# Optimization experiments

Measured on AMD Instinct MI355X. Metric: run time of the kernel, lower is better.

Reference implementation:

```python
import jax, jax.numpy as jnp
import numpy as np

B, L, D, H, NB = 64, 30, 512, 8, 6
AS, MT = 18, 4096
T = 3 * L
HD = D // H
EPS = 1e-3  # keras LayerNormalization default epsilon
CONV_FEAT = 7 * 7 * 64  # 84 ->(8,s4) 20 ->(4,s2) 9 ->(3,s1) 7


def setup_inputs() -> dict:
    key = jax.random.key(0)
    ks = iter(jax.random.split(key, 64))
    r = lambda *s: jax.random.normal(next(ks), s, jnp.float32) * 0.02
    inp = {
        'rtgs': jax.random.normal(next(ks), (B, L, 1), jnp.float32),
        'states': jax.random.uniform(next(ks), (B, L, 84, 84, 4), jnp.float32) * 255.0,
        'actions': jax.random.randint(next(ks), (B, L, 1), 0, AS),
        'timesteps': jax.random.randint(next(ks), (B, 1, 1), 0, MT + 1),
        # rtg embedding
        'W_rtg': r(1, D), 'b_rtg': r(D),
        # state conv stem (HWIO)
        'conv1_w': r(8, 8, 4, 32), 'conv1_b': r(32),
        'conv2_w': r(4, 4, 32, 64), 'conv2_b': r(64),
        'conv3_w': r(3, 3, 64, 64), 'conv3_b': r(64),
        'dense_s_w': r(CONV_FEAT, D), 'dense_s_b': r(D),
        # action embedding table
        'emb_a': r(AS, D),
        # positional embeddings
        'abs_pos': r(1, MT + 1, D), 'rel_pos': r(1, T + 1, D),
        # decoder blocks (stacked over NB)
        'ln1_g': 1.0 + r(NB, D), 'ln1_b': r(NB, D),
        'Wk': r(NB, D, D), 'bk': r(NB, D),
        'Wq': r(NB, D, D), 'bq': r(NB, D),
        'Wv': r(NB, D, D), 'bv': r(NB, D),
        'ln2_g': 1.0 + r(NB, D), 'ln2_b': r(NB, D),
        'W1': r(NB, D, 4 * D), 'b1': r(NB, 4 * D),
        'W2': r(NB, 4 * D, D), 'b2': r(NB, D),
        # final norm + head (no bias)
        'lnf_g': 1.0 + r(D), 'lnf_b': r(D),
        'W_head': r(D, AS),
    }
    return inp


def _conv(x, w, b, stride):
    y = jax.lax.conv_general_dilated(x, w, (stride, stride), 'VALID',
                                     dimension_numbers=('NHWC', 'HWIO', 'NHWC'))
    return jax.nn.relu(y + b)


def _layernorm(x, g, b):
    m = x.mean(-1, keepdims=True)
    v = ((x - m) ** 2).mean(-1, keepdims=True)
    return (x - m) / jnp.sqrt(v + EPS) * g + b


def _attn(x, Wk, bk, Wq, bq, Wv, bv):
    Bx, Tx, C = x.shape
    split = lambda z: z.reshape(Bx, Tx, H, HD).transpose(0, 2, 1, 3)  # (B,H,T,hd)
    k, q, v = split(x @ Wk + bk), split(x @ Wq + bq), split(x @ Wv + bv)
    # NOTE: faithful to source: scores = K @ Q^T (not Q @ K^T)
    s = jnp.einsum('bhid,bhjd->bhij', k, q) / jnp.sqrt(jnp.float32(HD))
    mask = jnp.tril(jnp.ones((Tx, Tx), bool))
    s = jnp.where(mask, s, -jnp.inf)
    w = jax.nn.softmax(s, axis=-1)
    o = jnp.einsum('bhij,bhjd->bhid', w, v)
    return o.transpose(0, 2, 1, 3).reshape(Bx, Tx, C)


def reference(rtgs, states, actions, timesteps, W_rtg, b_rtg,
              conv1_w, conv1_b, conv2_w, conv2_b, conv3_w, conv3_b,
              dense_s_w, dense_s_b, emb_a, abs_pos, rel_pos,
              ln1_g, ln1_b, Wk, bk, Wq, bq, Wv, bv,
              ln2_g, ln2_b, W1, b1, W2, b2, lnf_g, lnf_b, W_head):
    # embeddings
    rtg_e = jnp.tanh(rtgs @ W_rtg + b_rtg)                       # (B,L,D)
    s = states.reshape(B * L, 84, 84, 4) / 255.0
    s = _conv(s, conv1_w, conv1_b, 4)
    s = _conv(s, conv2_w, conv2_b, 2)
    s = _conv(s, conv3_w, conv3_b, 1)
    st_e = jnp.tanh(s.reshape(B, L, -1) @ dense_s_w + dense_s_b)  # (B,L,D)
    a_e = jnp.tanh(emb_a[actions[..., 0]])                        # (B,L,D)
    # positional: abs gathered at start timestep + relative
    abs_e = abs_pos[0][timesteps[:, 0, 0]][:, None, :]            # (B,1,D)
    pos = rel_pos[:, :T, :] + abs_e                               # (B,3L,D)
    # interleave (rtg, state, action) per timestep
    tokens = jnp.stack([rtg_e, st_e, a_e], axis=2).reshape(B, T, D)
    x = tokens + pos
    for i in range(NB):
        h = _layernorm(x, ln1_g[i], ln1_b[i])
        x = x + _attn(h, Wk[i], bk[i], Wq[i], bq[i], Wv[i], bv[i])
        h = _layernorm(x, ln2_g[i], ln2_b[i])
        x = x + jax.nn.gelu(h @ W1[i] + b1[i], approximate=False) @ W2[i] + b2[i]
    x = _layernorm(x, lnf_g, lnf_b)
    logits = x @ W_head                                           # (B,3L,AS)
    return logits[:, 1::3, :]                                     # state positions -> (B,L,AS)
```

## Files before the change

### kernel.cpp

```cpp
#include <hip/hip_runtime.h>
#include <hip/hip_bf16.h>

typedef __attribute__((ext_vector_type(8))) __bf16 bf16x8;
typedef __attribute__((ext_vector_type(4))) float f32x4;

#define ACT_NONE 0
#define ACT_RELU 1
#define ACT_GELU 2
#define ACT_TANH 3
#define OUT_F32 0
#define OUT_BF16 1
#define OUT_ADD 2

template<int MODE, int K>
__device__ __forceinline__ size_t a_rowbase(int m) {
  if constexpr (MODE == 0) {
    return (size_t)m * K;
  } else if constexpr (MODE == 1) {
    int img = m / 400; int p = m - img * 400; int oy = p / 20; int ox = p - oy * 20;
    return (size_t)img * 28224 + oy * 1344 + ox * 16;
  } else if constexpr (MODE == 2) {
    int img = m / 81; int p = m - img * 81; int oy = p / 9; int ox = p - oy * 9;
    return (size_t)img * 12800 + oy * 1280 + ox * 64;
  } else {
    int img = m / 49; int p = m - img * 49; int oy = p / 7; int ox = p - oy * 7;
    return (size_t)img * 5184 + oy * 576 + ox * 64;
  }
}
template<int MODE>
__device__ __forceinline__ int a_koff(int k) {
  if constexpr (MODE == 0) return k;
  else if constexpr (MODE == 1) return (k >> 5) * 336 + (k & 31);
  else if constexpr (MODE == 2) return (k >> 7) * 640 + ((k >> 5) & 3) * 32 + (k & 31);
  else { int ky = k / 192; int r = k - ky * 192; return ky * 576 + r; }
}

template<bool F32>
__device__ __forceinline__ bf16x8 ld8(const void* p) {
  if constexpr (F32) {
    const float* f = (const float*)p;
    float4 a = *(const float4*)f;
    float4 b = *(const float4*)(f + 4);
    bf16x8 r;
    r[0] = (__bf16)a.x; r[1] = (__bf16)a.y; r[2] = (__bf16)a.z; r[3] = (__bf16)a.w;
    r[4] = (__bf16)b.x; r[5] = (__bf16)b.y; r[6] = (__bf16)b.z; r[7] = (__bf16)b.w;
    return r;
  } else {
    return *(const bf16x8*)p;
  }
}

template<int MODE, bool AF32, int NREAL, int K, int ACT, int OUTM, int LDC>
__global__ __launch_bounds__(256) void gemm_k(const void* __restrict__ Av,
                                              const __bf16* __restrict__ BT,
                                              const float* __restrict__ bias,
                                              void* __restrict__ C) {
  constexpr int LDAS = 48;
  __shared__ __bf16 As[128 * LDAS];
  __shared__ __bf16 Bs[128 * LDAS];
  const __bf16* Ab = (const __bf16*)Av;
  const float* Af = (const float*)Av;
  const int tid = threadIdx.x;
  const int wave = tid >> 6, lane = tid & 63;
  const int quad = lane >> 4, l16 = lane & 15;
  const int wr = wave >> 1, wc = wave & 1;
  const int m0 = blockIdx.x * 128, n0 = blockIdx.y * 128;

  const int c0 = tid, c1 = tid + 256;
  const int r0 = c0 >> 2, k0o = (c0 & 3) * 8;
  const int r1 = c1 >> 2, k1o = (c1 & 3) * 8;
  const size_t ar0 = a_rowbase<MODE, K>(m0 + r0);
  const size_t ar1 = a_rowbase<MODE, K>(m0 + r1);
  const size_t br0 = (size_t)(n0 + r0) * K;
  const size_t br1 = (size_t)(n0 + r1) * K;

  auto aptr = [&](size_t idx) -> const void* {
    if constexpr (AF32) return (const void*)(Af + idx);
    else return (const void*)(Ab + idx);
  };

  f32x4 acc[4][4] = {};
  bf16x8 av0 = ld8<AF32>(aptr(ar0 + a_koff<MODE>(k0o)));
  bf16x8 av1 = ld8<AF32>(aptr(ar1 + a_koff<MODE>(k1o)));
  bf16x8 bv0 = *(const bf16x8*)(BT + br0 + k0o);
  bf16x8 bv1 = *(const bf16x8*)(BT + br1 + k1o);

  constexpr int NK = K / 32;
  for (int kt = 0; kt < NK; ++kt) {
    __syncthreads();
    *(bf16x8*)&As[r0 * LDAS + k0o] = av0;
    *(bf16x8*)&As[r1 * LDAS + k1o] = av1;
    *(bf16x8*)&Bs[r0 * LDAS + k0o] = bv0;
    *(bf16x8*)&Bs[r1 * LDAS + k1o] = bv1;
    __syncthreads();
    if (kt + 1 < NK) {
      const int kb = (kt + 1) * 32;
      av0 = ld8<AF32>(aptr(ar0 + a_koff<MODE>(kb + k0o)));
      av1 = ld8<AF32>(aptr(ar1 + a_koff<MODE>(kb + k1o)));
      bv0 = *(const bf16x8*)(BT + br0 + kb + k0o);
      bv1 = *(const bf16x8*)(BT + br1 + kb + k1o);
    }
    bf16x8 af[4], bfv[4];
#pragma unroll
    for (int mt = 0; mt < 4; ++mt)
      af[mt] = *(const bf16x8*)&As[(wr * 64 + mt * 16 + l16) * LDAS + quad * 8];
#pragma unroll
    for (int nt = 0; nt < 4; ++nt)
      bfv[nt] = *(const bf16x8*)&Bs[(wc * 64 + nt * 16 + l16) * LDAS + quad * 8];
#pragma unroll
    for (int mt = 0; mt < 4; ++mt)
#pragma unroll
      for (int nt = 0; nt < 4; ++nt)
        acc[mt][nt] = __builtin_amdgcn_mfma_f32_16x16x32_bf16(af[mt], bfv[nt], acc[mt][nt], 0, 0, 0);
  }

#pragma unroll
  for (int nt = 0; nt < 4; ++nt) {
    const int col = n0 + wc * 64 + nt * 16 + l16;
    if (col < NREAL) {
      const float bvl = bias[col];
#pragma unroll
      for (int mt = 0; mt < 4; ++mt) {
#pragma unroll
        for (int r = 0; r < 4; ++r) {
          const int row = m0 + wr * 64 + mt * 16 + quad * 4 + r;
          float v = acc[mt][nt][r] + bvl;
          if constexpr (ACT == ACT_RELU) v = fmaxf(v, 0.f);
          else if constexpr (ACT == ACT_GELU) v = 0.5f * v * (1.f + erff(v * 0.70710678118f));
          else if constexpr (ACT == ACT_TANH) v = tanhf(v);
          const size_t off = (size_t)row * LDC + col;
          if constexpr (OUTM == OUT_F32) ((float*)C)[off] = v;
          else if constexpr (OUTM == OUT_BF16) ((__bf16*)C)[off] = (__bf16)v;
          else ((float*)C)[off] += v;
        }
      }
    }
  }
}

template<typename TO>
__global__ void transpose_pad(const float* __restrict__ src, TO* __restrict__ dst,
                              int R, int C, int Cpad, long long sz, long long dz, float scale) {
  src += blockIdx.z * sz; dst += blockIdx.z * dz;
  __shared__ float t[32][33];
  const int tx = threadIdx.x, ty = threadIdx.y;
  const int r0 = blockIdx.x * 32, c0 = blockIdx.y * 32;
  for (int i = ty; i < 32; i += 8) {
    int r = r0 + i, c = c0 + tx;
    t[i][tx] = (r < R && c < C) ? src[(size_t)r * C + c] : 0.f;
  }
  __syncthreads();
  for (int i = ty; i < 32; i += 8) {
    int c = c0 + i, r = r0 + tx;
    if (c < Cpad && r < R)
      dst[(size_t)c * R + r] = (c < C) ? (TO)(t[tx][i] * scale) : (TO)0.f;
  }
}

__global__ void biascat_k(const float* bk, const float* bq, const float* bv, float* dst) {
  const int i = blockIdx.x;
  for (int d = threadIdx.x; d < 512; d += 256) {
    dst[i * 1536 + d] = bk[i * 512 + d];
    dst[i * 1536 + 512 + d] = bq[i * 512 + d];
    dst[i * 1536 + 1024 + d] = bv[i * 512 + d];
  }
}

__global__ void embed_k(const float* __restrict__ rtgs, const int* __restrict__ actions,
                        const int* __restrict__ timesteps, const float* __restrict__ W_rtg,
                        const float* __restrict__ b_rtg, const float* __restrict__ emb_a,
                        const float* __restrict__ abs_pos, const float* __restrict__ rel_pos,
                        const float* __restrict__ ste, float* __restrict__ x) {
  const int idx = blockIdx.x * 256 + threadIdx.x;
  const int d = idx & 511; const int rb = idx >> 9;
  const int b = rb / 90, t = rb - b * 90;
  const int l = t / 3, r = t - l * 3;
  const float pos = rel_pos[t * 512 + d] + abs_pos[(size_t)timesteps[b] * 512 + d];
  float tok;
  if (r == 0) tok = tanhf(rtgs[b * 30 + l] * W_rtg[d] + b_rtg[d]);
  else if (r == 1) tok = ste[(size_t)(b * 30 + l) * 512 + d];
  else tok = tanhf(emb_a[actions[b * 30 + l] * 512 + d]);
  x[idx] = tok + pos;
}

__global__ __launch_bounds__(256) void ln_k(const float* __restrict__ x, const float* __restrict__ g,
                                            const float* __restrict__ bb, __bf16* __restrict__ h) {
  const int row = blockIdx.x * 4 + (threadIdx.x >> 6);
  const int lane = threadIdx.x & 63;
  const float* xr = x + (size_t)row * 512;
  float4 a = *(const float4*)&xr[lane * 8];
  float4 c = *(const float4*)&xr[lane * 8 + 4];
  float vv[8] = {a.x, a.y, a.z, a.w, c.x, c.y, c.z, c.w};
  float s = 0.f, q = 0.f;
#pragma unroll
  for (int j = 0; j < 8; ++j) { s += vv[j]; q += vv[j] * vv[j]; }
  for (int o = 32; o; o >>= 1) { s += __shfl_xor(s, o); q += __shfl_xor(q, o); }
  const float mean = s * (1.f / 512.f);
  const float var = q * (1.f / 512.f) - mean * mean;
  const float rstd = rsqrtf(var + 1e-3f);
  float4 g1 = *(const float4*)&g[lane * 8];
  float4 g2 = *(const float4*)&g[lane * 8 + 4];
  float4 b1 = *(const float4*)&bb[lane * 8];
  float4 b2 = *(const float4*)&bb[lane * 8 + 4];
  float gg[8] = {g1.x, g1.y, g1.z, g1.w, g2.x, g2.y, g2.z, g2.w};
  float bbv[8] = {b1.x, b1.y, b1.z, b1.w, b2.x, b2.y, b2.z, b2.w};
  bf16x8 ov;
#pragma unroll
  for (int j = 0; j < 8; ++j)
    ov[j] = (__bf16)((vv[j] - mean) * rstd * gg[j] + bbv[j]);
  *(bf16x8*)&h[(size_t)row * 512 + lane * 8] = ov;
}

__global__ __launch_bounds__(256) void attn_k(const __bf16* __restrict__ qkv, float* __restrict__ x) {
  __shared__ __align__(16) char smem[64512];
  __bf16* kS = (__bf16*)smem;
  __bf16* qS = (__bf16*)(smem + 13824);
  __bf16* wS = (__bf16*)smem;
  float* sS = (float*)(smem + 27648);
  __bf16* vT = (__bf16*)(smem + 27648);

  const int tid = threadIdx.x;
  const int b = blockIdx.x >> 3, h = blockIdx.x & 7;
  const int wave = tid >> 6, lane = tid & 63, quad = lane >> 4, l16 = lane & 15;
  const size_t rowbase = (size_t)b * 90 * 1536 + h * 64;

  for (int c = tid; c < 768; c += 256) {
    const int t = c >> 3, d8 = (c & 7) * 8;
    bf16x8 kv, qv;
#pragma unroll
    for (int j = 0; j < 8; ++j) { kv[j] = (__bf16)0.f; qv[j] = (__bf16)0.f; }
    if (t < 90) {
      const __bf16* src = qkv + rowbase + (size_t)t * 1536 + d8;
      kv = *(const bf16x8*)src;
      qv = *(const bf16x8*)(src + 512);
    }
    *(bf16x8*)&kS[t * 72 + d8] = kv;
    *(bf16x8*)&qS[t * 72 + d8] = qv;
  }
  __syncthreads();

  for (int tt = wave; tt < 36; tt += 4) {
    const int it = tt / 6, jt = tt - it * 6;
    f32x4 acc = {0.f, 0.f, 0.f, 0.f};
#pragma unroll
    for (int ks = 0; ks < 2; ++ks) {
      bf16x8 af = *(const bf16x8*)&kS[(it * 16 + l16) * 72 + ks * 32 + quad * 8];
      bf16x8 bq = *(const bf16x8*)&qS[(jt * 16 + l16) * 72 + ks * 32 + quad * 8];
      acc = __builtin_amdgcn_mfma_f32_16x16x32_bf16(af, bq, acc, 0, 0, 0);
    }
    const int col = jt * 16 + l16;
#pragma unroll
    for (int r = 0; r < 4; ++r) {
      const int row = it * 16 + quad * 4 + r;
      sS[row * 96 + col] = (col <= row && col < 90) ? acc[r] * 0.125f : -1e30f;
    }
  }
  __syncthreads();

  for (int row = wave; row < 96; row += 4) {
    const float e0 = sS[row * 96 + lane];
    const float e1 = (lane < 32) ? sS[row * 96 + 64 + lane] : -1e30f;
    float m = fmaxf(e0, e1);
    for (int o = 32; o; o >>= 1) m = fmaxf(m, __shfl_xor(m, o));
    const float p0 = __expf(e0 - m);
    const float p1 = (lane < 32) ? __expf(e1 - m) : 0.f;
    float s = p0 + p1;
    for (int o = 32; o; o >>= 1) s += __shfl_xor(s, o);
    const float inv = 1.f / s;
    wS[row * 104 + lane] = (__bf16)(p0 * inv);
    if (lane < 32) wS[row * 104 + 64 + lane] = (__bf16)(p1 * inv);
  }
  __syncthreads();

  for (int c = tid; c < 768; c += 256) {
    const int t = c >> 3, d8 = (c & 7) * 8;
    bf16x8 vv;
#pragma unroll
    for (int j = 0; j < 8; ++j) vv[j] = (__bf16)0.f;
    if (t < 90) vv = *(const bf16x8*)(qkv + rowbase + (size_t)t * 1536 + 1024 + d8);
#pragma unroll
    for (int j = 0; j < 8; ++j) vT[(d8 + j) * 104 + t] = vv[j];
  }
  __syncthreads();

  for (int tt = wave; tt < 24; tt += 4) {
    const int it = tt >> 2, dt = tt & 3;
    f32x4 acc = {0.f, 0.f, 0.f, 0.f};
#pragma unroll
    for (int ks = 0; ks < 3; ++ks) {
      bf16x8 aw = *(const bf16x8*)&wS[(it * 16 + l16) * 104 + ks * 32 + quad * 8];
      bf16x8 bv = *(const bf16x8*)&vT[(dt * 16 + l16) * 104 + ks * 32 + quad * 8];
      acc = __builtin_amdgcn_mfma_f32_16x16x32_bf16(aw, bv, acc, 0, 0, 0);
    }
    const int d = dt * 16 + l16;
#pragma unroll
    for (int r = 0; r < 4; ++r) {
      const int i = it * 16 + quad * 4 + r;
      if (i < 90) {
        float* p = x + (size_t)(b * 90 + i) * 512 + h * 64 + d;
        *p += acc[r];
      }
    }
  }
}

__global__ __launch_bounds__(64) void head_k(const float* __restrict__ x, const float* __restrict__ g,
                                             const float* __restrict__ bb, const float* __restrict__ whT,
                                             float* __restrict__ out) {
  const int m = blockIdx.x;
  const int b = m / 30, l = m - b * 30;
  const float* xr = x + (size_t)(b * 90 + 3 * l + 1) * 512;
  const int lane = threadIdx.x;
  float4 a = *(const float4*)&xr[lane * 8];
  float4 c = *(const float4*)&xr[lane * 8 + 4];
  float vv[8] = {a.x, a.y, a.z, a.w, c.x, c.y, c.z, c.w};
  float s = 0.f, q = 0.f;
#pragma unroll
  for (int j = 0; j < 8; ++j) { s += vv[j]; q += vv[j] * vv[j]; }
  for (int o = 32; o; o >>= 1) { s += __shfl_xor(s, o); q += __shfl_xor(q, o); }
  const float mean = s * (1.f / 512.f);
  const float var = q * (1.f / 512.f) - mean * mean;
  const float rstd = rsqrtf(var + 1e-3f);
  float4 g1 = *(const float4*)&g[lane * 8];
  float4 g2 = *(const float4*)&g[lane * 8 + 4];
  float4 b1 = *(const float4*)&bb[lane * 8];
  float4 b2 = *(const float4*)&bb[lane * 8 + 4];
  float gg[8] = {g1.x, g1.y, g1.z, g1.w, g2.x, g2.y, g2.z, g2.w};
  float bbv[8] = {b1.x, b1.y, b1.z, b1.w, b2.x, b2.y, b2.z, b2.w};
#pragma unroll
  for (int j = 0; j < 8; ++j)
    vv[j] = (vv[j] - mean) * rstd * gg[j] + bbv[j];
  for (int aa = 0; aa < 18; ++aa) {
    float4 w1v = *(const float4*)&whT[aa * 512 + lane * 8];
    float4 w2v = *(const float4*)&whT[aa * 512 + lane * 8 + 4];
    float ww[8] = {w1v.x, w1v.y, w1v.z, w1v.w, w2v.x, w2v.y, w2v.z, w2v.w};
    float d = 0.f;
#pragma unroll
    for (int j = 0; j < 8; ++j) d += vv[j] * ww[j];
    for (int o = 32; o; o >>= 1) d += __shfl_xor(d, o);
    if (lane == 0) out[m * 18 + aa] = d;
  }
}

extern "C" void kernel_launch(void* const* d_in, const int* in_sizes, int n_in,
                              void* d_out, int out_size, void* d_ws, size_t ws_size,
                              hipStream_t stream) {
  const float* rtgs = (const float*)d_in[0];
  const float* states = (const float*)d_in[1];
  const int* actions = (const int*)d_in[2];
  const int* timesteps = (const int*)d_in[3];
  const float* W_rtg = (const float*)d_in[4];
  const float* b_rtg = (const float*)d_in[5];
  const float* conv1_w = (const float*)d_in[6];
  const float* conv1_b = (const float*)d_in[7];
  const float* conv2_w = (const float*)d_in[8];
  const float* conv2_b = (const float*)d_in[9];
  const float* conv3_w = (const float*)d_in[10];
  const float* conv3_b = (const float*)d_in[11];
  const float* dense_s_w = (const float*)d_in[12];
  const float* dense_s_b = (const float*)d_in[13];
  const float* emb_a = (const float*)d_in[14];
  const float* abs_pos = (const float*)d_in[15];
  const float* rel_pos = (const float*)d_in[16];
  const float* ln1_g = (const float*)d_in[17];
  const float* ln1_b = (const float*)d_in[18];
  const float* Wk = (const float*)d_in[19];
  const float* bk = (const float*)d_in[20];
  const float* Wq = (const float*)d_in[21];
  const float* bq = (const float*)d_in[22];
  const float* Wv = (const float*)d_in[23];
  const float* bv = (const float*)d_in[24];
  const float* ln2_g = (const float*)d_in[25];
  const float* ln2_b = (const float*)d_in[26];
  const float* W1 = (const float*)d_in[27];
  const float* b1 = (const float*)d_in[28];
  const float* W2 = (const float*)d_in[29];
  const float* b2 = (const float*)d_in[30];
  const float* lnf_g = (const float*)d_in[31];
  const float* lnf_b = (const float*)d_in[32];
  const float* W_head = (const float*)d_in[33];
  float* out = (float*)d_out;

  char* W = (char*)d_ws;
  float* x = (float*)(W + 0);
  __bf16* h = (__bf16*)(W + 11796480);
  __bf16* qkvT = (__bf16*)(W + 17694720);
  __bf16* w1T = (__bf16*)(W + 27131904);
  __bf16* w2T = (__bf16*)(W + 39714816);
  __bf16* dswT = (__bf16*)(W + 52297728);
  __bf16* c1wT = (__bf16*)(W + 55508992);
  __bf16* c2wT = (__bf16*)(W + 55574528);
  __bf16* c3wT = (__bf16*)(W + 55705600);
  float* whT = (float*)(W + 55853056);
  float* bqkv = (float*)(W + 55889920);
  __bf16* c1out = (__bf16*)(W + 55926784);
  __bf16* c2out = (__bf16*)(W + 105078784);
  __bf16* c3out = (__bf16*)(W + 55926784);
  float* ste = (float*)(W + 67969024);
  __bf16* qkvb = (__bf16*)(W + 55926784);
  __bf16* mlph = (__bf16*)(W + 73621504);

  const dim3 tb(32, 8);
  transpose_pad<__bf16><<<dim3(8, 4, 1), tb, 0, stream>>>(conv1_w, c1wT, 256, 32, 128, 0, 0, 1.f / 255.f);
  transpose_pad<__bf16><<<dim3(16, 4, 1), tb, 0, stream>>>(conv2_w, c2wT, 512, 64, 128, 0, 0, 1.f);
  transpose_pad<__bf16><<<dim3(18, 4, 1), tb, 0, stream>>>(conv3_w, c3wT, 576, 64, 128, 0, 0, 1.f);
  transpose_pad<__bf16><<<dim3(98, 16, 1), tb, 0, stream>>>(dense_s_w, dswT, 3136, 512, 512, 0, 0, 1.f);
  transpose_pad<__bf16><<<dim3(16, 16, 6), tb, 0, stream>>>(Wk, qkvT, 512, 512, 512, 512 * 512, 1536 * 512, 1.f);
  transpose_pad<__bf16><<<dim3(16, 16, 6), tb, 0, stream>>>(Wq, qkvT + 512 * 512, 512, 512, 512, 512 * 512, 1536 * 512, 1.f);
  transpose_pad<__bf16><<<dim3(16, 16, 6), tb, 0, stream>>>(Wv, qkvT + 1024 * 512, 512, 512, 512, 512 * 512, 1536 * 512, 1.f);
  transpose_pad<__bf16><<<dim3(16, 64, 6), tb, 0, stream>>>(W1, w1T, 512, 2048, 2048, 512 * 2048, 2048 * 512, 1.f);
  transpose_pad<__bf16><<<dim3(64, 16, 6), tb, 0, stream>>>(W2, w2T, 2048, 512, 512, 2048 * 512, 512 * 2048, 1.f);
  transpose_pad<float><<<dim3(16, 1, 1), tb, 0, stream>>>(W_head, whT, 512, 18, 18, 0, 0, 1.f);
  biascat_k<<<6, 256, 0, stream>>>(bk, bq, bv, bqkv);

  gemm_k<1, true, 32, 256, ACT_RELU, OUT_BF16, 32><<<dim3(6000, 1), 256, 0, stream>>>(states, c1wT, conv1_b, c1out);
  gemm_k<2, false, 64, 512, ACT_RELU, OUT_BF16, 64><<<dim3(1215, 1), 256, 0, stream>>>(c1out, c2wT, conv2_b, c2out);
  gemm_k<3, false, 64, 576, ACT_RELU, OUT_BF16, 64><<<dim3(735, 1), 256, 0, stream>>>(c2out, c3wT, conv3_b, c3out);
  gemm_k<0, false, 512, 3136, ACT_TANH, OUT_F32, 512><<<dim3(15, 4), 256, 0, stream>>>(c3out, dswT, dense_s_b, ste);

  embed_k<<<11520, 256, 0, stream>>>(rtgs, actions, timesteps, W_rtg, b_rtg, emb_a, abs_pos, rel_pos, ste, x);

  for (int i = 0; i < 6; ++i) {
    ln_k<<<1440, 256, 0, stream>>>(x, ln1_g + i * 512, ln1_b + i * 512, h);
    gemm_k<0, false, 1536, 512, ACT_NONE, OUT_BF16, 1536><<<dim3(45, 12), 256, 0, stream>>>(
        h, qkvT + (size_t)i * 1536 * 512, bqkv + i * 1536, qkvb);
    attn_k<<<512, 256, 0, stream>>>(qkvb, x);
    ln_k<<<1440, 256, 0, stream>>>(x, ln2_g + i * 512, ln2_b + i * 512, h);
    gemm_k<0, false, 2048, 512, ACT_GELU, OUT_BF16, 2048><<<dim3(45, 16), 256, 0, stream>>>(
        h, w1T + (size_t)i * 2048 * 512, b1 + i * 2048, mlph);
    gemm_k<0, false, 512, 2048, ACT_NONE, OUT_ADD, 512><<<dim3(45, 4), 256, 0, stream>>>(
        mlph, w2T + (size_t)i * 2048 * 512, b2 + i * 512, x);
  }

  head_k<<<1920, 64, 0, stream>>>(x, lnf_g, lnf_b, whT, out);
}
```

Measured before the change: 1.523 ms.

## Load GEMM tiles via global_load_lds, templatize tile shapes, add dedicated conv1 kernel

The GEMM kernel now loads A and B tiles straight into LDS with global_load_lds (16B per lane), which removes the register staging and software prefetch. Tile sizes and warp layouts become template parameters, and conv1 moves to its own 32-column kernel. The dense_s and W2 GEMMs get smaller tiles so more blocks are launched. The trade-offs are losing the register prefetch overlap and using an unpadded 32-element LDS row stride, which may cause bank conflicts.

Measured after the change: 1.392 ms. 1.09x faster.

```diff
diff --git a/kernel.cpp b/kernel.cpp
--- a/kernel.cpp
+++ b/kernel.cpp
@@ -11,6 +11,15 @@
 #define OUT_F32 0
 #define OUT_BF16 1
 #define OUT_ADD 2
+
+__device__ __forceinline__ void gll16(const void* g, void* l) {
+  __builtin_amdgcn_global_load_lds(
+      reinterpret_cast<const __attribute__((address_space(1))) unsigned int*>(
+          reinterpret_cast<unsigned long long>(g)),
+      reinterpret_cast<__attribute__((address_space(3))) unsigned int*>(
+          reinterpret_cast<unsigned long long>(l)),
+      16, 0, 0);
+}
 
 template<int MODE, int K>
 __device__ __forceinline__ size_t a_rowbase(int m) {
@@ -28,111 +37,154 @@
   }
 }
 template<int MODE>
-__device__ __forceinline__ int a_koff(int k) {
-  if constexpr (MODE == 0) return k;
-  else if constexpr (MODE == 1) return (k >> 5) * 336 + (k & 31);
-  else if constexpr (MODE == 2) return (k >> 7) * 640 + ((k >> 5) & 3) * 32 + (k & 31);
-  else { int ky = k / 192; int r = k - ky * 192; return ky * 576 + r; }
-}
-
-template<bool F32>
-__device__ __forceinline__ bf16x8 ld8(const void* p) {
-  if constexpr (F32) {
-    const float* f = (const float*)p;
-    float4 a = *(const float4*)f;
-    float4 b = *(const float4*)(f + 4);
-    bf16x8 r;
-    r[0] = (__bf16)a.x; r[1] = (__bf16)a.y; r[2] = (__bf16)a.z; r[3] = (__bf16)a.w;
-    r[4] = (__bf16)b.x; r[5] = (__bf16)b.y; r[6] = (__bf16)b.z; r[7] = (__bf16)b.w;
-    return r;
-  } else {
-    return *(const bf16x8*)p;
-  }
-}
-
-template<int MODE, bool AF32, int NREAL, int K, int ACT, int OUTM, int LDC>
-__global__ __launch_bounds__(256) void gemm_k(const void* __restrict__ Av,
+__device__ __forceinline__ int f_koff(int kb) {
+  if constexpr (MODE == 0) return kb;
+  else if constexpr (MODE == 2) return (kb >> 7) * 640 + ((kb >> 5) & 3) * 32;
+  else return kb + (kb / 192) * 384;
+}
+
+__device__ __forceinline__ bf16x8 ld8f(const float* f) {
+  float4 a = *(const float4*)f;
+  float4 b = *(const float4*)(f + 4);
+  bf16x8 r;
+  r[0] = (__bf16)a.x; r[1] = (__bf16)a.y; r[2] = (__bf16)a.z; r[3] = (__bf16)a.w;
+  r[4] = (__bf16)b.x; r[5] = (__bf16)b.y; r[6] = (__bf16)b.z; r[7] = (__bf16)b.w;
+  return r;
+}
+
+__device__ __forceinline__ float act_apply(float v, int ACT) {
+  if (ACT == ACT_RELU) return fmaxf(v, 0.f);
+  if (ACT == ACT_GELU) return 0.5f * v * (1.f + erff(v * 0.70710678118f));
+  if (ACT == ACT_TANH) return tanhf(v);
+  return v;
+}
+
+template<int MODE, int TM, int TN, int WM, int WN, int K, int ACT, int OUTM, int LDC>
+__global__ __launch_bounds__(256) void gemm_k(const __bf16* __restrict__ A,
                                               const __bf16* __restrict__ BT,
                                               const float* __restrict__ bias,
                                               void* __restrict__ C) {
-  constexpr int LDAS = 48;
-  __shared__ __bf16 As[128 * LDAS];
-  __shared__ __bf16 Bs[128 * LDAS];
-  const __bf16* Ab = (const __bf16*)Av;
-  const float* Af = (const float*)Av;
+  constexpr int SM = TM / WM, SN = TN / WN;
+  constexpr int AM = SM / 16, AN = SN / 16;
+  constexpr int TA = TM / 64, TB = TN / 64;
+  __shared__ __align__(16) __bf16 As[TM * 32];
+  __shared__ __align__(16) __bf16 Bs[TN * 32];
   const int tid = threadIdx.x;
   const int wave = tid >> 6, lane = tid & 63;
   const int quad = lane >> 4, l16 = lane & 15;
-  const int wr = wave >> 1, wc = wave & 1;
-  const int m0 = blockIdx.x * 128, n0 = blockIdx.y * 128;
-
-  const int c0 = tid, c1 = tid + 256;
-  const int r0 = c0 >> 2, k0o = (c0 & 3) * 8;
-  const int r1 = c1 >> 2, k1o = (c1 & 3) * 8;
-  const size_t ar0 = a_rowbase<MODE, K>(m0 + r0);
-  const size_t ar1 = a_rowbase<MODE, K>(m0 + r1);
-  const size_t br0 = (size_t)(n0 + r0) * K;
-  const size_t br1 = (size_t)(n0 + r1) * K;
-
-  auto aptr = [&](size_t idx) -> const void* {
-    if constexpr (AF32) return (const void*)(Af + idx);
-    else return (const void*)(Ab + idx);
-  };
-
-  f32x4 acc[4][4] = {};
-  bf16x8 av0 = ld8<AF32>(aptr(ar0 + a_koff<MODE>(k0o)));
-  bf16x8 av1 = ld8<AF32>(aptr(ar1 + a_koff<MODE>(k1o)));
-  bf16x8 bv0 = *(const bf16x8*)(BT + br0 + k0o);
-  bf16x8 bv1 = *(const bf16x8*)(BT + br1 + k1o);
-
-  constexpr int NK = K / 32;
-  for (int kt = 0; kt < NK; ++kt) {
+  const int wr = wave % WM, wc = wave / WM;
+  const int m0 = blockIdx.x * TM, n0 = blockIdx.y * TN;
+  const int lrow = lane >> 2, lkc = lane & 3;
+
+  const __bf16* ga[TA];
+  const __bf16* gb[TB];
+#pragma unroll
+  for (int t = 0; t < TA; ++t)
+    ga[t] = A + a_rowbase<MODE, K>(m0 + (wave + 4 * t) * 16 + lrow) + lkc * 8;
+#pragma unroll
+  for (int t = 0; t < TB; ++t)
+    gb[t] = BT + (size_t)(n0 + (wave + 4 * t) * 16 + lrow) * K + lkc * 8;
+
+  f32x4 acc[AM][AN] = {};
+  for (int kt = 0; kt < K / 32; ++kt) {
+    const int kb = kt * 32;
+    const int fa = f_koff<MODE>(kb);
     __syncthreads();
-    *(bf16x8*)&As[r0 * LDAS + k0o] = av0;
-    *(bf16x8*)&As[r1 * LDAS + k1o] = av1;
-    *(bf16x8*)&Bs[r0 * LDAS + k0o] = bv0;
-    *(bf16x8*)&Bs[r1 * LDAS + k1o] = bv1;
+#pragma unroll
+    for (int t = 0; t < TA; ++t)
+      gll16(ga[t] + fa, &As[(wave + 4 * t) * 16 * 32]);
+#pragma unroll
+    for (int t = 0; t < TB; ++t)
+      gll16(gb[t] + kb, &Bs[(wave + 4 * t) * 16 * 32]);
     __syncthreads();
-    if (kt + 1 < NK) {
-      const int kb = (kt + 1) * 32;
-      av0 = ld8<AF32>(aptr(ar0 + a_koff<MODE>(kb + k0o)));
-      av1 = ld8<AF32>(aptr(ar1 + a_koff<MODE>(kb + k1o)));
-      bv0 = *(const bf16x8*)(BT + br0 + kb + k0o);
-      bv1 = *(const bf16x8*)(BT + br1 + kb + k1o);
-    }
-    bf16x8 af[4], bfv[4];
-#pragma unroll
-    for (int mt = 0; mt < 4; ++mt)
-      af[mt] = *(const bf16x8*)&As[(wr * 64 + mt * 16 + l16) * LDAS + quad * 8];
-#pragma unroll
-    for (int nt = 0; nt < 4; ++nt)
-      bfv[nt] = *(const bf16x8*)&Bs[(wc * 64 + nt * 16 + l16) * LDAS + quad * 8];
-#pragma unroll
-    for (int mt = 0; mt < 4; ++mt)
-#pragma unroll
-      for (int nt = 0; nt < 4; ++nt)
-        acc[mt][nt] = __builtin_amdgcn_mfma_f32_16x16x32_bf16(af[mt], bfv[nt], acc[mt][nt], 0, 0, 0);
-  }
-
-#pragma unroll
-  for (int nt = 0; nt < 4; ++nt) {
-    const int col = n0 + wc * 64 + nt * 16 + l16;
-    if (col < NREAL) {
-      const float bvl = bias[col];
-#pragma unroll
-      for (int mt = 0; mt < 4; ++mt) {
-#pragma unroll
-        for (int r = 0; r < 4; ++r) {
-          const int row = m0 + wr * 64 + mt * 16 + quad * 4 + r;
-          float v = acc[mt][nt][r] + bvl;
-          if constexpr (ACT == ACT_RELU) v = fmaxf(v, 0.f);
-          else if constexpr (ACT == ACT_GELU) v = 0.5f * v * (1.f + erff(v * 0.70710678118f));
-          else if constexpr (ACT == ACT_TANH) v = tanhf(v);
-          const size_t off = (size_t)row * LDC + col;
-          if constexpr (OUTM == OUT_F32) ((float*)C)[off] = v;
-          else if constexpr (OUTM == OUT_BF16) ((__bf16*)C)[off] = (__bf16)v;
-          else ((float*)C)[off] += v;
-        }
+    bf16x8 af[AM], bf[AN];
+#pragma unroll
+    for (int mt = 0; mt < AM; ++mt)
+      af[mt] = *(const bf16x8*)&As[(wr * SM + mt * 16 + l16) * 32 + quad * 8];
+#pragma unroll
+    for (int nt = 0; nt < AN; ++nt)
+      bf[nt] = *(const bf16x8*)&Bs[(wc * SN + nt * 16 + l16) * 32 + quad * 8];
+#pragma unroll
+    for (int mt = 0; mt < AM; ++mt)
+#pragma unroll
+      for (int nt = 0; nt < AN; ++nt)
+        acc[mt][nt] = __builtin_amdgcn_mfma_f32_16x16x32_bf16(af[mt], bf[nt], acc[mt][nt], 0, 0, 0);
+  }
+
+#pragma unroll
+  for (int nt = 0; nt < AN; ++nt) {
+    const int col = n0 + wc * SN + nt * 16 + l16;
+    const float bvl = bias[col];
+#pragma unroll
+    for (int mt = 0; mt < AM; ++mt) {
+#pragma unroll
+      for (int r = 0; r < 4; ++r) {
+        const int row = m0 + wr * SM + mt * 16 + quad * 4 + r;
+        float v = act_apply(acc[mt][nt][r] + bvl, ACT);
+        const size_t off = (size_t)row * LDC + col;
+        if constexpr (OUTM == OUT_F32) ((float*)C)[off] = v;
+        else if constexpr (OUTM == OUT_BF16) ((__bf16*)C)[off] = (__bf16)v;
+        else ((float*)C)[off] += v;
+      }
+    }
+  }
+}
+
+__global__ __launch_bounds__(256) void conv1_k(const float* __restrict__ A,
+                                               const __bf16* __restrict__ BT,
+                                               const float* __restrict__ bias,
+                                               __bf16* __restrict__ C) {
+  __shared__ __align__(16) __bf16 As[128 * 32];
+  __shared__ __align__(16) __bf16 Bs[32 * 32];
+  const int tid = threadIdx.x;
+  const int wave = tid >> 6, lane = tid & 63;
+  const int quad = lane >> 4, l16 = lane & 15;
+  const int m0 = blockIdx.x * 128;
+  const int lrow = lane >> 2, lkc = lane & 3;
+  const int r0 = tid >> 2, k0o = (tid & 3) * 8;
+  const int r1 = r0 + 64;
+  const size_t ar0 = a_rowbase<1, 256>(m0 + r0);
+  const size_t ar1 = a_rowbase<1, 256>(m0 + r1);
+  const __bf16* gB = BT + (size_t)(wave * 16 + lrow) * 256 + lkc * 8;
+
+  f32x4 acc[2][2] = {};
+  bf16x8 a0 = ld8f(A + ar0 + k0o);
+  bf16x8 a1 = ld8f(A + ar1 + k0o);
+  for (int kt = 0; kt < 8; ++kt) {
+    const int kb = kt * 32;
+    __syncthreads();
+    if (wave < 2) gll16(gB + kb, &Bs[wave * 16 * 32]);
+    *(bf16x8*)&As[r0 * 32 + k0o] = a0;
+    *(bf16x8*)&As[r1 * 32 + k0o] = a1;
+    __syncthreads();
+    if (kt < 7) {
+      const int fa = (kt + 1) * 336;
+      a0 = ld8f(A + ar0 + fa + k0o);
+      a1 = ld8f(A + ar1 + fa + k0o);
+    }
+    bf16x8 af[2], bf[2];
+#pragma unroll
+    for (int mt = 0; mt < 2; ++mt)
+      af[mt] = *(const bf16x8*)&As[(wave * 32 + mt * 16 + l16) * 32 + quad * 8];
+#pragma unroll
+    for (int nt = 0; nt < 2; ++nt)
+      bf[nt] = *(const bf16x8*)&Bs[(nt * 16 + l16) * 32 + quad * 8];
+#pragma unroll
+    for (int mt = 0; mt < 2; ++mt)
+#pragma unroll
+      for (int nt = 0; nt < 2; ++nt)
+        acc[mt][nt] = __builtin_amdgcn_mfma_f32_16x16x32_bf16(af[mt], bf[nt], acc[mt][nt], 0, 0, 0);
+  }
+#pragma unroll
+  for (int nt = 0; nt < 2; ++nt) {
+    const int col = nt * 16 + l16;
+    const float bvl = bias[col];
+#pragma unroll
+    for (int mt = 0; mt < 2; ++mt) {
+#pragma unroll
+      for (int r = 0; r < 4; ++r) {
+        const int row = m0 + wave * 32 + mt * 16 + quad * 4 + r;
+        C[(size_t)row * 32 + col] = (__bf16)fmaxf(acc[mt][nt][r] + bvl, 0.f);
       }
     }
   }
@@ -413,22 +465,22 @@
   transpose_pad<float><<<dim3(16, 1, 1), tb, 0, stream>>>(W_head, whT, 512, 18, 18, 0, 0, 1.f);
   biascat_k<<<6, 256, 0, stream>>>(bk, bq, bv, bqkv);
 
-  gemm_k<1, true, 32, 256, ACT_RELU, OUT_BF16, 32><<<dim3(6000, 1), 256, 0, stream>>>(states, c1wT, conv1_b, c1out);
-  gemm_k<2, false, 64, 512, ACT_RELU, OUT_BF16, 64><<<dim3(1215, 1), 256, 0, stream>>>(c1out, c2wT, conv2_b, c2out);
-  gemm_k<3, false, 64, 576, ACT_RELU, OUT_BF16, 64><<<dim3(735, 1), 256, 0, stream>>>(c2out, c3wT, conv3_b, c3out);
-  gemm_k<0, false, 512, 3136, ACT_TANH, OUT_F32, 512><<<dim3(15, 4), 256, 0, stream>>>(c3out, dswT, dense_s_b, ste);
+  conv1_k<<<6000, 256, 0, stream>>>(states, c1wT, conv1_b, c1out);
+  gemm_k<2, 128, 64, 2, 2, 512, ACT_RELU, OUT_BF16, 64><<<dim3(1215, 1), 256, 0, stream>>>(c1out, c2wT, conv2_b, c2out);
+  gemm_k<3, 128, 64, 2, 2, 576, ACT_RELU, OUT_BF16, 64><<<dim3(735, 1), 256, 0, stream>>>(c2out, c3wT, conv3_b, c3out);
+  gemm_k<0, 64, 64, 2, 2, 3136, ACT_TANH, OUT_F32, 512><<<dim3(30, 8), 256, 0, stream>>>(c3out, dswT, dense_s_b, (void*)ste);
 
   embed_k<<<11520, 256, 0, stream>>>(rtgs, actions, timesteps, W_rtg, b_rtg, emb_a, abs_pos, rel_pos, ste, x);
 
   for (int i = 0; i < 6; ++i) {
     ln_k<<<1440, 256, 0, stream>>>(x, ln1_g + i * 512, ln1_b + i * 512, h);
-    gemm_k<0, false, 1536, 512, ACT_NONE, OUT_BF16, 1536><<<dim3(45, 12), 256, 0, stream>>>(
+    gemm_k<0, 128, 128, 2, 2, 512, ACT_NONE, OUT_BF16, 1536><<<dim3(45, 12), 256, 0, stream>>>(
         h, qkvT + (size_t)i * 1536 * 512, bqkv + i * 1536, qkvb);
     attn_k<<<512, 256, 0, stream>>>(qkvb, x);
     ln_k<<<1440, 256, 0, stream>>>(x, ln2_g + i * 512, ln2_b + i * 512, h);
-    gemm_k<0, false, 2048, 512, ACT_GELU, OUT_BF16, 2048><<<dim3(45, 16), 256, 0, stream>>>(
+    gemm_k<0, 128, 128, 2, 2, 512, ACT_GELU, OUT_BF16, 2048><<<dim3(45, 16), 256, 0, stream>>>(
         h, w1T + (size_t)i * 2048 * 512, b1 + i * 2048, mlph);
-    gemm_k<0, false, 512, 2048, ACT_NONE, OUT_ADD, 512><<<dim3(45, 4), 256, 0, stream>>>(
+    gemm_k<0, 64, 128, 2, 2, 2048, ACT_NONE, OUT_ADD, 512><<<dim3(90, 4), 256, 0, stream>>>(
         mlph, w2T + (size_t)i * 2048 * 512, b2 + i * 512, x);
   }
 
```
